# Kernel optimization log

Hardware: AMD Instinct MI355X
Metric: run time of the kernel (lower is better)

## Reference

```python
import jax, jax.numpy as jnp
import numpy as np

# scipy.ndimage.gaussian_filter(sigma=1, truncate=4): radius 4, 9-tap kernel on EVERY axis
_R = 4
_xk = np.arange(-_R, _R + 1)
_wk = np.exp(-0.5 * _xk * _xk)
_W1D = (_wk / _wk.sum()).astype(np.float32)


def _sym_idx(n, r):
    # scipy 'reflect' (symmetric, edge repeated) extension indices for any r, any n
    p = np.arange(-r, n + r)
    q = np.mod(p, 2 * n)
    return np.where(q < n, q, 2 * n - 1 - q)


def gauss_filter(x):
    # separable sigma=1 Gaussian over ALL axes (incl. batch & channel), as scipy does
    w = jnp.asarray(_W1D)
    for axis in range(x.ndim):
        n = x.shape[axis]
        idx = jnp.asarray(_sym_idx(n, _R))
        xp = jnp.take(x, idx, axis=axis)  # symmetric-padded along `axis`
        acc = w[0] * jax.lax.slice_in_dim(xp, 0, n, axis=axis)
        for k in range(1, 2 * _R + 1):
            acc = acc + w[k] * jax.lax.slice_in_dim(xp, k, k + n, axis=axis)
        x = acc
    return x


def downsample(x):
    return x[:, :, ::2, ::2, ::2]


def upsample(x):
    # faithful to source: zero-interleave D and H, but zeros are APPENDED along W
    B, C, D, H, W = x.shape
    t = jnp.stack([x, jnp.zeros_like(x)], axis=3).reshape(B, C, 2 * D, H, W)
    t = jnp.stack([t, jnp.zeros_like(t)], axis=4).reshape(B, C, 2 * D, 2 * H, W)
    t = jnp.concatenate([t, jnp.zeros_like(t)], axis=4)  # (B,C,2D,2H,2W), 2nd W-half zero
    return gauss_filter(t * 8.0)


def lap_pyramid(img, max_levels):
    pyr = []
    cur = img
    for _ in range(max_levels):
        filt = gauss_filter(cur)
        down = downsample(filt)
        up = upsample(down)
        pyr.append(cur - up)
        cur = down
    return pyr


def setup_inputs():
    key = jax.random.key(0)
    k1, k2 = jax.random.split(key)
    shape = (2, 1, 64, 256, 256)
    return {
        "input": jax.random.normal(k1, shape, dtype=jnp.float32),
        "target": jax.random.normal(k2, shape, dtype=jnp.float32),
    }


def reference(input, target):
    max_levels = 5
    pyr_in = lap_pyramid(input, max_levels)
    pyr_tg = lap_pyramid(target, max_levels)
    loss = jnp.float32(0.0)
    for a, b in zip(pyr_in, pyr_tg):
        loss = loss + jnp.mean(jnp.abs(a - b))  # F.l1_loss (mean reduction)
    return loss
```

## Files before the change

kernel.cpp:

```cpp
#include <hip/hip_runtime.h>
#include <hip/hip_bf16.h>
#include <math.h>


struct GW { float w[9]; float A, B; };

__device__ __forceinline__ int ridx(int p, int n) {
    int m = 2 * n;
    int q = (p + m) & (m - 1);
    return (q < n) ? q : (m - 1 - q);
}

__device__ __forceinline__ float block_sum256(float v) {
    #pragma unroll
    for (int off = 32; off > 0; off >>= 1) v += __shfl_down(v, off, 64);
    __shared__ float wp[4];
    int tid = threadIdx.x;
    if ((tid & 63) == 0) wp[tid >> 6] = v;
    __syncthreads();
    return wp[0] + wp[1] + wp[2] + wp[3];
}

template<bool WDIFF>
__global__ __launch_bounds__(256)
void k1l0(const float* __restrict__ in, const float* __restrict__ tg,
          float* __restrict__ T1, __hip_bfloat16* __restrict__ DIFF,
          float* __restrict__ P, GW g)
{
    const int H = 256, W = 256, Wd = 128;
    const int x0d = blockIdx.x * 64, y0d = blockIdx.y * 16, slice = blockIdx.z;
    __shared__ float raw[40][136];
    __shared__ float mid[40][64];
    const size_t in_off  = (size_t)slice * H * W;
    const size_t out_off = (size_t)slice * 128 * 128;
    const int tid = threadIdx.x;
    const int gy0 = 2*y0d - 4, gx0 = 2*x0d - 4;
    for (int i = tid; i < 40*32; i += 256) {
        int rr = i >> 5, c4 = (i & 31) + 1;
        int gy = ridx(gy0 + rr, H);
        size_t base = in_off + (size_t)gy * W + gx0 + 4*c4;
        float4 v = *(const float4*)(in + base);
        float4 b = *(const float4*)(tg + base);
        v.x -= b.x; v.y -= b.y; v.z -= b.z; v.w -= b.w;
        *(float4*)&raw[rr][4*c4] = v;
    }
    for (int i = tid; i < 40*8; i += 256) {
        int rr = i >> 3, j = i & 7;
        int cc = (j < 4) ? j : (128 + j);
        int gy = ridx(gy0 + rr, H);
        int gx = ridx(gx0 + cc, W);
        size_t idx = in_off + (size_t)gy * W + gx;
        raw[rr][cc] = in[idx] - tg[idx];
    }
    __syncthreads();
    if (WDIFF) {
        if (blockIdx.x == 0) {
            for (int i = tid; i < 32*128; i += 256) {
                int r = i >> 7, c = i & 127;
                DIFF[in_off + (size_t)(2*y0d + r) * W + c] =
                    __float2bfloat16(raw[4 + r][4 + c]);
            }
        } else {
            for (int i = tid; i < 32*4; i += 256) {
                int r = i >> 2, c = i & 3;
                DIFF[in_off + (size_t)(2*y0d + r) * W + 128 + c] =
                    __float2bfloat16(raw[4 + r][4 + c]);
            }
        }
    }
    if (blockIdx.x == 1) {
        float lsum = 0.f;
        for (int i = tid; i < 32*124; i += 256) {
            int r = i / 124, c = i - r*124;
            lsum += fabsf(raw[4 + r][8 + c]);
        }
        float tot = block_sum256(lsum);
        if (tid == 0)
            P[blockIdx.y + 8*blockIdx.z] = tot * (1.f / 8388608.f);
    }
    for (int i = tid; i < 40*64; i += 256) {
        int rr = i >> 6, c = i & 63;
        float s = 0.f;
        #pragma unroll
        for (int k = 0; k < 9; ++k) s = fmaf(g.w[k], raw[rr][2*c + k], s);
        mid[rr][c] = s;
    }
    __syncthreads();
    {
        int r = tid >> 6, c = tid & 63;
        int ox = x0d + c;
        #pragma unroll
        for (int j = 0; j < 4; ++j) {
            int oy = y0d + r*4 + j;
            int rb = 2*(r*4 + j);
            float s = 0.f;
            #pragma unroll
            for (int k = 0; k < 9; ++k) s = fmaf(g.w[k], mid[rb + k][c], s);
            T1[out_off + (size_t)oy * Wd + ox] = s;
        }
    }
}

__global__ __launch_bounds__(256)
void k2s(const float* __restrict__ Tin, float* __restrict__ Cout,
         int D, int Dd, int M4, GW g)
{
    long i = (long)blockIdx.x * 256 + threadIdx.x;
    if (i >= (long)Dd * M4) return;
    int zd = (int)(i / M4);
    int q  = (int)(i - (long)zd * M4);
    const float4* T = (const float4*)Tin;
    float4* O = (float4*)Cout;
    float4 s0 = {0,0,0,0}, s1 = {0,0,0,0};
    #pragma unroll
    for (int k = 0; k < 9; ++k) {
        int zp = 2*zd - 4 + k;
        int zk = (zp >= 0 && zp < D) ? zp : ridx(zp, D);
        float4 a = T[(size_t)zk * M4 + q];
        float4 b = T[(size_t)(D + zk) * M4 + q];
        s0.x = fmaf(g.w[k], a.x, s0.x); s0.y = fmaf(g.w[k], a.y, s0.y);
        s0.z = fmaf(g.w[k], a.z, s0.z); s0.w = fmaf(g.w[k], a.w, s0.w);
        s1.x = fmaf(g.w[k], b.x, s1.x); s1.y = fmaf(g.w[k], b.y, s1.y);
        s1.z = fmaf(g.w[k], b.z, s1.z); s1.w = fmaf(g.w[k], b.w, s1.w);
    }
    float4 o0, o1;
    o0.x = g.A*s0.x + g.B*s1.x; o0.y = g.A*s0.y + g.B*s1.y;
    o0.z = g.A*s0.z + g.B*s1.z; o0.w = g.A*s0.w + g.B*s1.w;
    o1.x = g.B*s0.x + g.A*s1.x; o1.y = g.B*s0.y + g.A*s1.y;
    o1.z = g.B*s0.z + g.A*s1.z; o1.w = g.B*s0.w + g.A*s1.w;
    O[(size_t)zd * M4 + q] = o0;
    O[(size_t)(Dd + zd) * M4 + q] = o1;
}

__device__ void dev_k1_slice(const float* __restrict__ inA, float* __restrict__ out,
                             int x0d, int y0d, int slice, int H, int W, int Hd, int Wd,
                             const GW& g)
{
    __shared__ float raw[40][136];
    __shared__ float mid[40][64];
    const size_t in_off  = (size_t)slice * H * W;
    const size_t out_off = (size_t)slice * Hd * Wd;
    const int tid = threadIdx.x;
    const int gy0 = 2*y0d - 4, gx0 = 2*x0d - 4;
    if (2*x0d + 127 < W) {
        for (int i = tid; i < 40*32; i += 256) {
            int rr = i >> 5, c4 = (i & 31) + 1;
            int gy = ridx(gy0 + rr, H);
            *(float4*)&raw[rr][4*c4] =
                *(const float4*)(inA + in_off + (size_t)gy * W + gx0 + 4*c4);
        }
        for (int i = tid; i < 40*8; i += 256) {
            int rr = i >> 3, j = i & 7;
            int cc = (j < 4) ? j : (128 + j);
            int gy = ridx(gy0 + rr, H), gx = ridx(gx0 + cc, W);
            raw[rr][cc] = inA[in_off + (size_t)gy * W + gx];
        }
    } else {
        for (int i = tid; i < 40*136; i += 256) {
            int rr = i / 136, cc = i - rr*136;
            int gy = ridx(gy0 + rr, H), gx = ridx(gx0 + cc, W);
            raw[rr][cc] = inA[in_off + (size_t)gy * W + gx];
        }
    }
    __syncthreads();
    for (int i = tid; i < 40*64; i += 256) {
        int rr = i >> 6, c = i & 63;
        float s = 0.f;
        #pragma unroll
        for (int k = 0; k < 9; ++k) s = fmaf(g.w[k], raw[rr][2*c + k], s);
        mid[rr][c] = s;
    }
    __syncthreads();
    {
        int r = tid >> 6, c = tid & 63;
        int ox = x0d + c;
        #pragma unroll
        for (int j = 0; j < 4; ++j) {
            int oy = y0d + r*4 + j;
            if (oy < Hd && ox < Wd) {
                int rb = 2*(r*4 + j);
                float s = 0.f;
                #pragma unroll
                for (int k = 0; k < 9; ++k) s = fmaf(g.w[k], mid[rb + k][c], s);
                out[out_off + (size_t)oy * Wd + ox] = s;
            }
        }
    }
}

__global__ __launch_bounds__(256)
void k1s(const float* __restrict__ inA, float* __restrict__ out,
         int H, int W, int Hd, int Wd, GW g)
{
    dev_k1_slice(inA, out, blockIdx.x*64, blockIdx.y*16, blockIdx.z, H, W, Hd, Wd, g);
}

__device__ void dev_k3_elem(long i, const float4* __restrict__ Dn, float4* __restrict__ O,
                            int D, int Dd, int M4, const GW& g)
{
    if (i >= (long)D * M4) return;
    int z = (int)(i / M4);
    int q = (int)(i - (long)z * M4);
    float4 s0 = {0,0,0,0}, s1 = {0,0,0,0};
    auto f4 = [](float4& a, float w, const float4 b) {
        a.x = fmaf(w, b.x, a.x); a.y = fmaf(w, b.y, a.y);
        a.z = fmaf(w, b.z, a.z); a.w = fmaf(w, b.w, a.w);
    };
    if (z >= 4 && z + 4 < D) {
        if ((z & 1) == 0) {
            int base = (z >> 1) - 2;
            #pragma unroll
            for (int kk = 0; kk < 5; ++kk) {
                f4(s0, g.w[2*kk], Dn[(size_t)(base + kk) * M4 + q]);
                f4(s1, g.w[2*kk], Dn[(size_t)(Dd + base + kk) * M4 + q]);
            }
        } else {
            int base = (z - 3) >> 1;
            #pragma unroll
            for (int kk = 0; kk < 4; ++kk) {
                f4(s0, g.w[2*kk+1], Dn[(size_t)(base + kk) * M4 + q]);
                f4(s1, g.w[2*kk+1], Dn[(size_t)(Dd + base + kk) * M4 + q]);
            }
        }
    } else {
        #pragma unroll
        for (int k = 0; k < 9; ++k) {
            int zk = ridx(z - 4 + k, D);
            if (!(zk & 1)) {
                int j = zk >> 1;
                f4(s0, g.w[k], Dn[(size_t)j * M4 + q]);
                f4(s1, g.w[k], Dn[(size_t)(Dd + j) * M4 + q]);
            }
        }
    }
    float4 o0, o1;
    o0.x = 8.f*(g.A*s0.x + g.B*s1.x); o0.y = 8.f*(g.A*s0.y + g.B*s1.y);
    o0.z = 8.f*(g.A*s0.z + g.B*s1.z); o0.w = 8.f*(g.A*s0.w + g.B*s1.w);
    o1.x = 8.f*(g.B*s0.x + g.A*s1.x); o1.y = 8.f*(g.B*s0.y + g.A*s1.y);
    o1.z = 8.f*(g.B*s0.z + g.A*s1.z); o1.w = 8.f*(g.B*s0.w + g.A*s1.w);
    O[(size_t)z * M4 + q] = o0;
    O[(size_t)(D + z) * M4 + q] = o1;
}

__global__ __launch_bounds__(256)
void fatk(const float* __restrict__ k1in, float* __restrict__ k1out,
          int H, int W, int Hd, int Wd, int nty, int n1,
          const float* __restrict__ dn, float* __restrict__ V,
          int D, int Dd, int M4, GW g)
{
    if ((int)blockIdx.x < n1) {
        int ty = (int)blockIdx.x % nty, slice = (int)blockIdx.x / nty;
        dev_k1_slice(k1in, k1out, 0, ty*16, slice, H, W, Hd, Wd, g);
    } else {
        long i = (long)((int)blockIdx.x - n1)*256 + threadIdx.x;
        dev_k3_elem(i, (const float4*)dn, (float4*)V, D, Dd, M4, g);
    }
}

struct K4P {
    const float* V[3];
    const float* dn34[2];
    const float* cur[5];
    const float* in; const float* tg;
    const __hip_bfloat16* DIFF;
    float* P;
    int use_diff;
    int bo[6];
    GW g;
};

__global__ __launch_bounds__(256)
void k4all(K4P p)
{
    const int Dt[5] = {64,32,16,8,4}, Ht[5] = {256,128,64,32,16};
    __shared__ float vt[20][72];
    __shared__ float mid[20][64];
    const int bid = (int)blockIdx.x;
    int l = 0;
    while (l < 4 && bid >= p.bo[l+1]) ++l;
    const int local = bid - p.bo[l];
    const int D = Dt[l], H = Ht[l], W = H;
    const int Dd = D >> 1, Hd = H >> 1, Wd = W >> 1, Md = Hd * Wd;
    const int ntx = (l == 0) ? 3 : ((W + 63) >> 6);
    const int nty = (H + 31) >> 5;
    const int s = local / (ntx*nty);
    const int rem = local - s*(ntx*nty);
    const int ty = rem / ntx, tx = rem - ty*ntx;
    const int x0 = tx*64, y0 = ty*32;
    const int b = s / D, z = s - b*D;
    const GW g = p.g;
    const int tid = threadIdx.x;
    const int vy0 = (y0 >> 1) - 2;

    if (l < 3) {
        const float* V = p.V[l];
        const size_t v_off = (size_t)s * Md;
        for (int i = tid; i < 20*72; i += 256) {
            int rr = i / 72, cc = i - rr*72;
            int vy = vy0 + rr;
            int txx = x0 - 4 + cc;
            if (txx < 0) txx = -1 - txx;
            float v = 0.f;
            if (vy >= 0 && vy < Hd && txx < Wd) v = V[v_off + (size_t)vy * Wd + txx];
            vt[rr][cc] = v;
        }
    } else {
        const float* dnb = p.dn34[l-3];
        const float* dn0 = dnb + (size_t)b * Dd * Md;
        const float* dn1 = dnb + (size_t)(1 - b) * Dd * Md;
        for (int i = tid; i < 20*72; i += 256) {
            int rr = i / 72, cc = i - rr*72;
            int vy = vy0 + rr;
            int txx = x0 - 4 + cc;
            if (txx < 0) txx = -1 - txx;
            float v = 0.f;
            if (vy >= 0 && vy < Hd && txx < Wd) {
                size_t o = (size_t)vy * Wd + txx;
                float s0 = 0.f, s1 = 0.f;
                #pragma unroll
                for (int k = 0; k < 9; ++k) {
                    int zk = ridx(z - 4 + k, D);
                    if (!(zk & 1)) {
                        int j = zk >> 1;
                        s0 = fmaf(g.w[k], dn0[(size_t)j * Md + o], s0);
                        s1 = fmaf(g.w[k], dn1[(size_t)j * Md + o], s1);
                    }
                }
                v = 8.f * (g.A*s0 + g.B*s1);
            }
            vt[rr][cc] = v;
        }
    }
    __syncthreads();
    for (int i = tid; i < 20*64; i += 256) {
        int rr = i >> 6, c = i & 63;
        float sv = 0.f;
        #pragma unroll
        for (int k = 0; k < 9; ++k) sv = fmaf(g.w[k], vt[rr][c + k], sv);
        mid[rr][c] = sv;
    }
    __syncthreads();
    const bool yin = (y0 >= 4) && (y0 + 35 < H);
    const int c = tid & 63;
    const int ry_base = (tid >> 6) * 8;
    const int ox = x0 + c;
    const int xlim = (l == 0) ? 132 : W;
    const size_t c_off = (size_t)s * H * W;
    const float* curl = (l >= 1) ? p.cur[l] : nullptr;
    float lsum = 0.f;
    #pragma unroll
    for (int j = 0; j < 8; ++j) {
        int ry = ry_base + j;
        int oy = y0 + ry;
        if (ox < xlim && oy < H) {
            float sv = 0.f;
            if (yin) {
                if (!(j & 1)) {
                    int r0 = ry >> 1;
                    sv = g.w[0]*mid[r0][c] + g.w[2]*mid[r0+1][c] + g.w[4]*mid[r0+2][c]
                       + g.w[6]*mid[r0+3][c] + g.w[8]*mid[r0+4][c];
                } else {
                    int r0 = ((ry - 3) >> 1) + 2;
                    sv = g.w[1]*mid[r0][c] + g.w[3]*mid[r0+1][c]
                       + g.w[5]*mid[r0+2][c] + g.w[7]*mid[r0+3][c];
                }
            } else {
                #pragma unroll
                for (int k = 0; k < 9; ++k) {
                    int gy = ridx(oy - 4 + k, H);
                    if (!(gy & 1)) sv = fmaf(g.w[k], mid[(gy >> 1) - vy0][c], sv);
                }
            }
            size_t idx = c_off + (size_t)oy * W + ox;
            float cv;
            if (l == 0) cv = p.use_diff ? __bfloat162float(p.DIFF[idx])
                                        : (p.in[idx] - p.tg[idx]);
            else        cv = curl[idx];
            lsum += fabsf(cv - sv);
        }
    }
    float tot = block_sum256(lsum);
    if (tid == 0) p.P[1024 + bid] = tot / ((float)(2*D) * H * W);
}

__global__ __launch_bounds__(1024)
void kreduce(const float* __restrict__ P, int n, float* __restrict__ out)
{
    float s = 0.f;
    for (int i = threadIdx.x; i < n; i += 1024) s += P[i];
    #pragma unroll
    for (int off = 32; off > 0; off >>= 1) s += __shfl_down(s, off, 64);
    __shared__ float wp[16];
    if ((threadIdx.x & 63) == 0) wp[threadIdx.x >> 6] = s;
    __syncthreads();
    if (threadIdx.x == 0) {
        float t = 0.f;
        #pragma unroll
        for (int w = 0; w < 16; ++w) t += wp[w];
        out[0] = t;
    }
}

extern "C" void kernel_launch(void* const* d_in, const int* in_sizes, int n_in,
                              void* d_out, int out_size, void* d_ws, size_t ws_size,
                              hipStream_t stream)
{
    const float* in = (const float*)d_in[0];
    const float* tg = (const float*)d_in[1];
    float* out = (float*)d_out;

    GW g;
    {
        double u[9], S = 0.0;
        for (int k = 0; k < 9; ++k) { double d = k - 4; u[k] = exp(-0.5 * d * d); S += u[k]; }
        for (int k = 0; k < 9; ++k) g.w[k] = (float)(u[k] / S);
        g.A = (float)((2.0*u[0] + u[1] + u[3] + u[4]) / S);
        g.B = (float)((u[1] + 2.0*u[2] + u[3]) / S);
    }

    float* T1  = (float*)d_ws;
    float* C1  = T1  + 2097152;
    float* C2  = C1  + 1048576;
    float* C3  = C2  + 131072;
    float* C4  = C3  + 16384;
    float* C5  = C4  + 2048;
    float* Tl1 = C5  + 256;
    float* Tl2 = Tl1 + 262144;
    float* Tl3 = Tl2 + 32768;
    float* Tl4 = Tl3 + 4096;
    float* V0  = Tl4 + 512;
    float* V1  = V0  + 2097152;
    float* V2  = V1  + 262144;
    float* P   = V2  + 32768;
    float* wend = P + 8192;
    __hip_bfloat16* DIFF = (__hip_bfloat16*)wend;
    const size_t base_bytes = (size_t)((char*)wend - (char*)d_ws);
    const size_t diff_bytes = (size_t)2 * 64 * 256 * 256 * sizeof(__hip_bfloat16);
    const int use_diff = (ws_size >= base_bytes + diff_bytes) ? 1 : 0;

    dim3 blk(256);

    if (use_diff) k1l0<true ><<<dim3(2,8,128), blk, 0, stream>>>(in, tg, T1, DIFF, P, g);
    else          k1l0<false><<<dim3(2,8,128), blk, 0, stream>>>(in, tg, T1, nullptr, P, g);

    k2s<<<dim3(512), blk, 0, stream>>>(T1, C1, 64, 32, 4096, g);

    fatk<<<dim3(256 + 1024), blk, 0, stream>>>(C1, Tl1, 128, 128, 64, 64, 4, 256,
                                               C1, V0, 64, 32, 4096, g);
    k2s<<<dim3(64), blk, 0, stream>>>(Tl1, C2, 32, 16, 1024, g);

    fatk<<<dim3(64 + 128), blk, 0, stream>>>(C2, Tl2, 64, 64, 32, 32, 2, 64,
                                             C2, V1, 32, 16, 1024, g);
    k2s<<<dim3(8), blk, 0, stream>>>(Tl2, C3, 16, 8, 256, g);

    fatk<<<dim3(16 + 16), blk, 0, stream>>>(C3, Tl3, 32, 32, 16, 16, 1, 16,
                                            C3, V2, 16, 8, 256, g);
    k2s<<<dim3(1), blk, 0, stream>>>(Tl3, C4, 8, 4, 64, g);

    k1s<<<dim3(1,1,8), blk, 0, stream>>>(C4, Tl4, 16, 16, 8, 8, g);
    k2s<<<dim3(1), blk, 0, stream>>>(Tl4, C5, 4, 2, 16, g);

    K4P prm;
    prm.V[0] = V0; prm.V[1] = V1; prm.V[2] = V2;
    prm.dn34[0] = C4; prm.dn34[1] = C5;
    prm.cur[0] = nullptr; prm.cur[1] = C1; prm.cur[2] = C2; prm.cur[3] = C3; prm.cur[4] = C4;
    prm.in = in; prm.tg = tg;
    prm.DIFF = use_diff ? DIFF : nullptr;
    prm.P = P; prm.use_diff = use_diff;
    prm.g = g;
    prm.bo[0] = 0; prm.bo[1] = 3072; prm.bo[2] = 3584;
    prm.bo[3] = 3648; prm.bo[4] = 3664; prm.bo[5] = 3672;
    k4all<<<dim3(3672), blk, 0, stream>>>(prm);

    kreduce<<<1, 1024, 0, stream>>>(P, 1024 + 3672, out);
}
```

Measured before the change: 102.2 us.

## Fuse depth pass into next level's H/W filter and interleave loss blocks

Folds the separate depth/batch filter kernels (k2s) into the next level's in-plane filter kernel. Each block now computes the D-axis and batch-axis Gaussian while loading its tile, stores the downsampled level, and then runs the H/W passes. The per-level loss kernel is split into chunks that share launches with the later small stages, cutting the launch count and the serial dependency chain. The cost is redundant D-filter work on halo rows and scalar (non-float4) strided loads, and the merged kernels use a larger shared-memory footprint, which can lower occupancy for the loss blocks.

```diff
diff --git a/kernel.cpp b/kernel.cpp
--- a/kernel.cpp
+++ b/kernel.cpp
@@ -101,103 +101,77 @@
     }
 }
 
-__global__ __launch_bounds__(256)
-void k2s(const float* __restrict__ Tin, float* __restrict__ Cout,
-         int D, int Dd, int M4, GW g)
-{
-    long i = (long)blockIdx.x * 256 + threadIdx.x;
-    if (i >= (long)Dd * M4) return;
-    int zd = (int)(i / M4);
-    int q  = (int)(i - (long)zd * M4);
-    const float4* T = (const float4*)Tin;
-    float4* O = (float4*)Cout;
-    float4 s0 = {0,0,0,0}, s1 = {0,0,0,0};
-    #pragma unroll
-    for (int k = 0; k < 9; ++k) {
-        int zp = 2*zd - 4 + k;
-        int zk = (zp >= 0 && zp < D) ? zp : ridx(zp, D);
-        float4 a = T[(size_t)zk * M4 + q];
-        float4 b = T[(size_t)(D + zk) * M4 + q];
-        s0.x = fmaf(g.w[k], a.x, s0.x); s0.y = fmaf(g.w[k], a.y, s0.y);
-        s0.z = fmaf(g.w[k], a.z, s0.z); s0.w = fmaf(g.w[k], a.w, s0.w);
-        s1.x = fmaf(g.w[k], b.x, s1.x); s1.y = fmaf(g.w[k], b.y, s1.y);
-        s1.z = fmaf(g.w[k], b.z, s1.z); s1.w = fmaf(g.w[k], b.w, s1.w);
-    }
-    float4 o0, o1;
-    o0.x = g.A*s0.x + g.B*s1.x; o0.y = g.A*s0.y + g.B*s1.y;
-    o0.z = g.A*s0.z + g.B*s1.z; o0.w = g.A*s0.w + g.B*s1.w;
-    o1.x = g.B*s0.x + g.A*s1.x; o1.y = g.B*s0.y + g.A*s1.y;
-    o1.z = g.B*s0.z + g.A*s1.z; o1.w = g.B*s0.w + g.A*s1.w;
-    O[(size_t)zd * M4 + q] = o0;
-    O[(size_t)(Dd + zd) * M4 + q] = o1;
-}
-
-__device__ void dev_k1_slice(const float* __restrict__ inA, float* __restrict__ out,
-                             int x0d, int y0d, int slice, int H, int W, int Hd, int Wd,
-                             const GW& g)
-{
-    __shared__ float raw[40][136];
-    __shared__ float mid[40][64];
-    const size_t in_off  = (size_t)slice * H * W;
-    const size_t out_off = (size_t)slice * Hd * Wd;
+struct MP {
+    const float* Tin; float* C; float* Tout;
+    int Dz, Dc, Hp, Wp, nty, writeT, nM;
+};
+
+__device__ void dev_M(int m, const MP& mp, const GW& g, float* smem)
+{
+    float* raw = smem;
+    float* mid = smem + 40*136;
     const int tid = threadIdx.x;
-    const int gy0 = 2*y0d - 4, gx0 = 2*x0d - 4;
-    if (2*x0d + 127 < W) {
-        for (int i = tid; i < 40*32; i += 256) {
-            int rr = i >> 5, c4 = (i & 31) + 1;
-            int gy = ridx(gy0 + rr, H);
-            *(float4*)&raw[rr][4*c4] =
-                *(const float4*)(inA + in_off + (size_t)gy * W + gx0 + 4*c4);
-        }
-        for (int i = tid; i < 40*8; i += 256) {
-            int rr = i >> 3, j = i & 7;
-            int cc = (j < 4) ? j : (128 + j);
-            int gy = ridx(gy0 + rr, H), gx = ridx(gx0 + cc, W);
-            raw[rr][cc] = inA[in_off + (size_t)gy * W + gx];
-        }
-    } else {
-        for (int i = tid; i < 40*136; i += 256) {
-            int rr = i / 136, cc = i - rr*136;
-            int gy = ridx(gy0 + rr, H), gx = ridx(gx0 + cc, W);
-            raw[rr][cc] = inA[in_off + (size_t)gy * W + gx];
-        }
-    }
+    const int ytile = m % mp.nty;
+    const int zidx  = m / mp.nty;
+    const int b  = zidx / mp.Dc;
+    const int zc = zidx - b * mp.Dc;
+    const int Dz = mp.Dz, Hp = mp.Hp, Wp = mp.Wp;
+    const int Hd = Hp >> 1, Wd = Wp >> 1;
+    const int y0d = ytile * 16;
+    const int CC = (Wp + 8 > 136) ? 136 : (Wp + 8);
+    const size_t plane = (size_t)Hp * Wp;
+    for (int i = tid; i < 40*CC; i += 256) {
+        int rr = i / CC, cc = i - rr*CC;
+        int gy = ridx(2*y0d - 4 + rr, Hp);
+        int gx = ridx(cc - 4, Wp);
+        size_t base = (size_t)gy * Wp + gx;
+        float s0 = 0.f, s1 = 0.f;
+        #pragma unroll
+        for (int k = 0; k < 9; ++k) {
+            int zt = ridx(2*zc - 4 + k, Dz);
+            s0 = fmaf(g.w[k], mp.Tin[(size_t)zt * plane + base], s0);
+            s1 = fmaf(g.w[k], mp.Tin[(size_t)(Dz + zt) * plane + base], s1);
+        }
+        float val = (b == 0) ? (g.A*s0 + g.B*s1) : (g.B*s0 + g.A*s1);
+        raw[rr*136 + cc] = val;
+        int gyo = 2*y0d + rr - 4;
+        if (rr >= 4 && rr < 36 && gyo < Hp && cc >= 4 && cc < 4 + Wp) {
+            mp.C[((size_t)(b*mp.Dc + zc) * Hp + gyo) * Wp + (cc - 4)] = val;
+        }
+    }
+    if (!mp.writeT) return;
     __syncthreads();
     for (int i = tid; i < 40*64; i += 256) {
         int rr = i >> 6, c = i & 63;
         float s = 0.f;
         #pragma unroll
-        for (int k = 0; k < 9; ++k) s = fmaf(g.w[k], raw[rr][2*c + k], s);
-        mid[rr][c] = s;
+        for (int k = 0; k < 9; ++k) s = fmaf(g.w[k], raw[rr*136 + 2*c + k], s);
+        mid[rr*64 + c] = s;
     }
     __syncthreads();
     {
         int r = tid >> 6, c = tid & 63;
-        int ox = x0d + c;
         #pragma unroll
         for (int j = 0; j < 4; ++j) {
             int oy = y0d + r*4 + j;
-            if (oy < Hd && ox < Wd) {
+            if (oy < Hd && c < Wd) {
                 int rb = 2*(r*4 + j);
                 float s = 0.f;
                 #pragma unroll
-                for (int k = 0; k < 9; ++k) s = fmaf(g.w[k], mid[rb + k][c], s);
-                out[out_off + (size_t)oy * Wd + ox] = s;
-            }
-        }
-    }
-}
-
-__global__ __launch_bounds__(256)
-void k1s(const float* __restrict__ inA, float* __restrict__ out,
-         int H, int W, int Hd, int Wd, GW g)
-{
-    dev_k1_slice(inA, out, blockIdx.x*64, blockIdx.y*16, blockIdx.z, H, W, Hd, Wd, g);
-}
-
-__device__ void dev_k3_elem(long i, const float4* __restrict__ Dn, float4* __restrict__ O,
-                            int D, int Dd, int M4, const GW& g)
-{
+                for (int k = 0; k < 9; ++k) s = fmaf(g.w[k], mid[(rb+k)*64 + c], s);
+                mp.Tout[((size_t)(b*mp.Dc + zc) * Hd + oy) * Wd + c] = s;
+            }
+        }
+    }
+}
+
+struct K3 { const float* dn; float* V; int D, Dd, M4, n; };
+
+__device__ void dev_k3_elem(long i, const K3& kp, const GW& g)
+{
+    const float4* Dn = (const float4*)kp.dn;
+    float4* O = (float4*)kp.V;
+    const int D = kp.D, Dd = kp.Dd, M4 = kp.M4;
     if (i >= (long)D * M4) return;
     int z = (int)(i / M4);
     int q = (int)(i - (long)z * M4);
@@ -242,21 +216,6 @@
     O[(size_t)(D + z) * M4 + q] = o1;
 }
 
-__global__ __launch_bounds__(256)
-void fatk(const float* __restrict__ k1in, float* __restrict__ k1out,
-          int H, int W, int Hd, int Wd, int nty, int n1,
-          const float* __restrict__ dn, float* __restrict__ V,
-          int D, int Dd, int M4, GW g)
-{
-    if ((int)blockIdx.x < n1) {
-        int ty = (int)blockIdx.x % nty, slice = (int)blockIdx.x / nty;
-        dev_k1_slice(k1in, k1out, 0, ty*16, slice, H, W, Hd, Wd, g);
-    } else {
-        long i = (long)((int)blockIdx.x - n1)*256 + threadIdx.x;
-        dev_k3_elem(i, (const float4*)dn, (float4*)V, D, Dd, M4, g);
-    }
-}
-
 struct K4P {
     const float* V[3];
     const float* dn34[2];
@@ -269,16 +228,14 @@
     GW g;
 };
 
-__global__ __launch_bounds__(256)
-void k4all(K4P p)
+__device__ void dev_k4(int gbid, const K4P& p, float* smem)
 {
     const int Dt[5] = {64,32,16,8,4}, Ht[5] = {256,128,64,32,16};
-    __shared__ float vt[20][72];
-    __shared__ float mid[20][64];
-    const int bid = (int)blockIdx.x;
+    float* vt  = smem;
+    float* mid = smem + 20*72;
     int l = 0;
-    while (l < 4 && bid >= p.bo[l+1]) ++l;
-    const int local = bid - p.bo[l];
+    while (l < 4 && gbid >= p.bo[l+1]) ++l;
+    const int local = gbid - p.bo[l];
     const int D = Dt[l], H = Ht[l], W = H;
     const int Dd = D >> 1, Hd = H >> 1, Wd = W >> 1, Md = Hd * Wd;
     const int ntx = (l == 0) ? 3 : ((W + 63) >> 6);
@@ -302,7 +259,7 @@
             if (txx < 0) txx = -1 - txx;
             float v = 0.f;
             if (vy >= 0 && vy < Hd && txx < Wd) v = V[v_off + (size_t)vy * Wd + txx];
-            vt[rr][cc] = v;
+            vt[rr*72 + cc] = v;
         }
     } else {
         const float* dnb = p.dn34[l-3];
@@ -328,7 +285,7 @@
                 }
                 v = 8.f * (g.A*s0 + g.B*s1);
             }
-            vt[rr][cc] = v;
+            vt[rr*72 + cc] = v;
         }
     }
     __syncthreads();
@@ -336,8 +293,8 @@
         int rr = i >> 6, c = i & 63;
         float sv = 0.f;
         #pragma unroll
-        for (int k = 0; k < 9; ++k) sv = fmaf(g.w[k], vt[rr][c + k], sv);
-        mid[rr][c] = sv;
+        for (int k = 0; k < 9; ++k) sv = fmaf(g.w[k], vt[rr*72 + c + k], sv);
+        mid[rr*64 + c] = sv;
     }
     __syncthreads();
     const bool yin = (y0 >= 4) && (y0 + 35 < H);
@@ -357,18 +314,19 @@
             if (yin) {
                 if (!(j & 1)) {
                     int r0 = ry >> 1;
-                    sv = g.w[0]*mid[r0][c] + g.w[2]*mid[r0+1][c] + g.w[4]*mid[r0+2][c]
-                       + g.w[6]*mid[r0+3][c] + g.w[8]*mid[r0+4][c];
+                    sv = g.w[0]*mid[r0*64+c] + g.w[2]*mid[(r0+1)*64+c]
+                       + g.w[4]*mid[(r0+2)*64+c] + g.w[6]*mid[(r0+3)*64+c]
+                       + g.w[8]*mid[(r0+4)*64+c];
                 } else {
                     int r0 = ((ry - 3) >> 1) + 2;
-                    sv = g.w[1]*mid[r0][c] + g.w[3]*mid[r0+1][c]
-                       + g.w[5]*mid[r0+2][c] + g.w[7]*mid[r0+3][c];
+                    sv = g.w[1]*mid[r0*64+c] + g.w[3]*mid[(r0+1)*64+c]
+                       + g.w[5]*mid[(r0+2)*64+c] + g.w[7]*mid[(r0+3)*64+c];
                 }
             } else {
                 #pragma unroll
                 for (int k = 0; k < 9; ++k) {
                     int gy = ridx(oy - 4 + k, H);
-                    if (!(gy & 1)) sv = fmaf(g.w[k], mid[(gy >> 1) - vy0][c], sv);
+                    if (!(gy & 1)) sv = fmaf(g.w[k], mid[((gy >> 1) - vy0)*64 + c], sv);
                 }
             }
             size_t idx = c_off + (size_t)oy * W + ox;
@@ -380,7 +338,50 @@
         }
     }
     float tot = block_sum256(lsum);
-    if (tid == 0) p.P[1024 + bid] = tot / ((float)(2*D) * H * W);
+    if (tid == 0) p.P[1024 + gbid] = tot / ((float)(2*D) * H * W);
+}
+
+__global__ __launch_bounds__(256)
+void kM1(MP mp, GW g)
+{
+    __shared__ float smem[40*136 + 40*64];
+    dev_M((int)blockIdx.x, mp, g, smem);
+}
+
+__global__ __launch_bounds__(256)
+void kD3(MP mp, K3 k3, GW g)
+{
+    __shared__ float smem[40*136 + 40*64];
+    int bid = (int)blockIdx.x;
+    if (bid < mp.nM) dev_M(bid, mp, g, smem);
+    else dev_k3_elem((long)(bid - mp.nM)*256 + threadIdx.x, k3, g);
+}
+
+__global__ __launch_bounds__(256)
+void kD45(MP mp, K3 k3, K4P k4, int bid0, GW g)
+{
+    __shared__ float smem[40*136 + 40*64];
+    int bid = (int)blockIdx.x;
+    if (bid < mp.nM) dev_M(bid, mp, g, smem);
+    else if (bid < mp.nM + k3.n)
+        dev_k3_elem((long)(bid - mp.nM)*256 + threadIdx.x, k3, g);
+    else dev_k4(bid0 + (bid - mp.nM - k3.n), k4, smem);
+}
+
+__global__ __launch_bounds__(256)
+void kD6(MP mp, K4P k4, int bid0, GW g)
+{
+    __shared__ float smem[40*136 + 40*64];
+    int bid = (int)blockIdx.x;
+    if (bid < mp.nM) dev_M(bid, mp, g, smem);
+    else dev_k4(bid0 + (bid - mp.nM), k4, smem);
+}
+
+__global__ __launch_bounds__(256)
+void kD7(K4P k4, int bid0)
+{
+    __shared__ float smem[20*72 + 20*64];
+    dev_k4(bid0 + (int)blockIdx.x, k4, smem);
 }
 
 __global__ __launch_bounds__(1024)
@@ -440,37 +441,54 @@
 
     dim3 blk(256);
 
+    K4P k4;
+    k4.V[0] = V0; k4.V[1] = V1; k4.V[2] = V2;
+    k4.dn34[0] = C4; k4.dn34[1] = C5;
+    k4.cur[0] = nullptr; k4.cur[1] = C1; k4.cur[2] = C2; k4.cur[3] = C3; k4.cur[4] = C4;
+    k4.in = in; k4.tg = tg;
+    k4.DIFF = use_diff ? DIFF : nullptr;
+    k4.P = P; k4.use_diff = use_diff;
+    k4.g = g;
+    k4.bo[0] = 0; k4.bo[1] = 3072; k4.bo[2] = 3584;
+    k4.bo[3] = 3648; k4.bo[4] = 3664; k4.bo[5] = 3672;
+
     if (use_diff) k1l0<true ><<<dim3(2,8,128), blk, 0, stream>>>(in, tg, T1, DIFF, P, g);
     else          k1l0<false><<<dim3(2,8,128), blk, 0, stream>>>(in, tg, T1, nullptr, P, g);
 
-    k2s<<<dim3(512), blk, 0, stream>>>(T1, C1, 64, 32, 4096, g);
-
-    fatk<<<dim3(256 + 1024), blk, 0, stream>>>(C1, Tl1, 128, 128, 64, 64, 4, 256,
-                                               C1, V0, 64, 32, 4096, g);
-    k2s<<<dim3(64), blk, 0, stream>>>(Tl1, C2, 32, 16, 1024, g);
-
-    fatk<<<dim3(64 + 128), blk, 0, stream>>>(C2, Tl2, 64, 64, 32, 32, 2, 64,
-                                             C2, V1, 32, 16, 1024, g);
-    k2s<<<dim3(8), blk, 0, stream>>>(Tl2, C3, 16, 8, 256, g);
-
-    fatk<<<dim3(16 + 16), blk, 0, stream>>>(C3, Tl3, 32, 32, 16, 16, 1, 16,
-                                            C3, V2, 16, 8, 256, g);
-    k2s<<<dim3(1), blk, 0, stream>>>(Tl3, C4, 8, 4, 64, g);
-
-    k1s<<<dim3(1,1,8), blk, 0, stream>>>(C4, Tl4, 16, 16, 8, 8, g);
-    k2s<<<dim3(1), blk, 0, stream>>>(Tl4, C5, 4, 2, 16, g);
-
-    K4P prm;
-    prm.V[0] = V0; prm.V[1] = V1; prm.V[2] = V2;
-    prm.dn34[0] = C4; prm.dn34[1] = C5;
-    prm.cur[0] = nullptr; prm.cur[1] = C1; prm.cur[2] = C2; prm.cur[3] = C3; prm.cur[4] = C4;
-    prm.in = in; prm.tg = tg;
-    prm.DIFF = use_diff ? DIFF : nullptr;
-    prm.P = P; prm.use_diff = use_diff;
-    prm.g = g;
-    prm.bo[0] = 0; prm.bo[1] = 3072; prm.bo[2] = 3584;
-    prm.bo[3] = 3648; prm.bo[4] = 3664; prm.bo[5] = 3672;
-    k4all<<<dim3(3672), blk, 0, stream>>>(prm);
+    {
+        MP mp; mp.Tin = T1; mp.C = C1; mp.Tout = Tl1;
+        mp.Dz = 64; mp.Dc = 32; mp.Hp = 128; mp.Wp = 128; mp.nty = 4; mp.writeT = 1;
+        mp.nM = 256;
+        kM1<<<dim3(256), blk, 0, stream>>>(mp, g);
+    }
+    {
+        MP mp; mp.Tin = Tl1; mp.C = C2; mp.Tout = Tl2;
+        mp.Dz = 32; mp.Dc = 16; mp.Hp = 64; mp.Wp = 64; mp.nty = 2; mp.writeT = 1;
+        mp.nM = 64;
+        K3 k3 = { C1, V0, 64, 32, 4096, 1024 };
+        kD3<<<dim3(64 + 1024), blk, 0, stream>>>(mp, k3, g);
+    }
+    {
+        MP mp; mp.Tin = Tl2; mp.C = C3; mp.Tout = Tl3;
+        mp.Dz = 16; mp.Dc = 8; mp.Hp = 32; mp.Wp = 32; mp.nty = 1; mp.writeT = 1;
+        mp.nM = 16;
+        K3 k3 = { C2, V1, 32, 16, 1024, 128 };
+        kD45<<<dim3(16 + 128 + 3072), blk, 0, stream>>>(mp, k3, k4, 0, g);
+    }
+    {
+        MP mp; mp.Tin = Tl3; mp.C = C4; mp.Tout = Tl4;
+        mp.Dz = 8; mp.Dc = 4; mp.Hp = 16; mp.Wp = 16; mp.nty = 1; mp.writeT = 1;
+        mp.nM = 8;
+        K3 k3 = { C3, V2, 16, 8, 256, 16 };
+        kD45<<<dim3(8 + 16 + 512), blk, 0, stream>>>(mp, k3, k4, 3072, g);
+    }
+    {
+        MP mp; mp.Tin = Tl4; mp.C = C5; mp.Tout = nullptr;
+        mp.Dz = 4; mp.Dc = 2; mp.Hp = 8; mp.Wp = 8; mp.nty = 1; mp.writeT = 0;
+        mp.nM = 4;
+        kD6<<<dim3(4 + 64), blk, 0, stream>>>(mp, k4, 3584, g);
+    }
+    kD7<<<dim3(24), blk, 0, stream>>>(k4, 3648);
 
     kreduce<<<1, 1024, 0, stream>>>(P, 1024 + 3672, out);
 }
```

Result: slower. 128.8 us (+26.0%).

## Restructure pyramid schedule: fuse level losses into producer kernels and single-block tail

Applied to the files above, without the earlier changes.

The launch sequence is reorganised so each level's loss computation runs in the same launch as the next level's filtering. Levels 1-2 compute the z-upsample directly from the downsampled data instead of materialising V1/V2, and all of levels 3-4 are collapsed into one 1024-thread block working from shared memory. This cuts the kernel launch count and the intermediate global traffic, and lets the large level-0 loss overlap with the small level-1 z-pass. In exchange, the tail runs serially on a single block, and levels 1-2 recompute the z-upsample per tile, including over halo rows.

```diff
diff --git a/kernel.cpp b/kernel.cpp
--- a/kernel.cpp
+++ b/kernel.cpp
@@ -19,6 +19,21 @@
     if ((tid & 63) == 0) wp[tid >> 6] = v;
     __syncthreads();
     return wp[0] + wp[1] + wp[2] + wp[3];
+}
+
+__device__ __forceinline__ float block_sum1024(float v) {
+    #pragma unroll
+    for (int off = 32; off > 0; off >>= 1) v += __shfl_down(v, off, 64);
+    __shared__ float wp[16];
+    int tid = threadIdx.x;
+    if ((tid & 63) == 0) wp[tid >> 6] = v;
+    __syncthreads();
+    float t = 0.f;
+    if (tid == 0) {
+        #pragma unroll
+        for (int w = 0; w < 16; ++w) t += wp[w];
+    }
+    return t;
 }
 
 template<bool WDIFF>
@@ -101,16 +116,12 @@
     }
 }
 
-__global__ __launch_bounds__(256)
-void k2s(const float* __restrict__ Tin, float* __restrict__ Cout,
-         int D, int Dd, int M4, GW g)
-{
-    long i = (long)blockIdx.x * 256 + threadIdx.x;
+__device__ void dev_k2_elem(long i, const float4* __restrict__ T, float4* __restrict__ O,
+                            int D, int Dd, int M4, const GW& g)
+{
     if (i >= (long)Dd * M4) return;
     int zd = (int)(i / M4);
     int q  = (int)(i - (long)zd * M4);
-    const float4* T = (const float4*)Tin;
-    float4* O = (float4*)Cout;
     float4 s0 = {0,0,0,0}, s1 = {0,0,0,0};
     #pragma unroll
     for (int k = 0; k < 9; ++k) {
@@ -130,6 +141,14 @@
     o1.z = g.B*s0.z + g.A*s1.z; o1.w = g.B*s0.w + g.A*s1.w;
     O[(size_t)zd * M4 + q] = o0;
     O[(size_t)(Dd + zd) * M4 + q] = o1;
+}
+
+__global__ __launch_bounds__(256)
+void k2s(const float* __restrict__ Tin, float* __restrict__ Cout,
+         int D, int Dd, int M4, GW g)
+{
+    long i = (long)blockIdx.x * 256 + threadIdx.x;
+    dev_k2_elem(i, (const float4*)Tin, (float4*)Cout, D, Dd, M4, g);
 }
 
 __device__ void dev_k1_slice(const float* __restrict__ inA, float* __restrict__ out,
@@ -186,13 +205,6 @@
             }
         }
     }
-}
-
-__global__ __launch_bounds__(256)
-void k1s(const float* __restrict__ inA, float* __restrict__ out,
-         int H, int W, int Hd, int Wd, GW g)
-{
-    dev_k1_slice(inA, out, blockIdx.x*64, blockIdx.y*16, blockIdx.z, H, W, Hd, Wd, g);
 }
 
 __device__ void dev_k3_elem(long i, const float4* __restrict__ Dn, float4* __restrict__ O,
@@ -242,72 +254,136 @@
     O[(size_t)(D + z) * M4 + q] = o1;
 }
 
-__global__ __launch_bounds__(256)
-void fatk(const float* __restrict__ k1in, float* __restrict__ k1out,
-          int H, int W, int Hd, int Wd, int nty, int n1,
-          const float* __restrict__ dn, float* __restrict__ V,
-          int D, int Dd, int M4, GW g)
-{
-    if ((int)blockIdx.x < n1) {
-        int ty = (int)blockIdx.x % nty, slice = (int)blockIdx.x / nty;
-        dev_k1_slice(k1in, k1out, 0, ty*16, slice, H, W, Hd, Wd, g);
-    } else {
-        long i = (long)((int)blockIdx.x - n1)*256 + threadIdx.x;
-        dev_k3_elem(i, (const float4*)dn, (float4*)V, D, Dd, M4, g);
-    }
-}
-
-struct K4P {
-    const float* V[3];
-    const float* dn34[2];
-    const float* cur[5];
-    const float* in; const float* tg;
-    const __hip_bfloat16* DIFF;
-    float* P;
-    int use_diff;
-    int bo[6];
-    GW g;
-};
-
-__global__ __launch_bounds__(256)
-void k4all(K4P p)
-{
-    const int Dt[5] = {64,32,16,8,4}, Ht[5] = {256,128,64,32,16};
+__device__ void dev_k4v0(int local, const float* __restrict__ V0,
+                         const __hip_bfloat16* __restrict__ DIFF,
+                         const float* __restrict__ in, const float* __restrict__ tg,
+                         int use_diff, float* __restrict__ P, const GW& g)
+{
     __shared__ float vt[20][72];
     __shared__ float mid[20][64];
-    const int bid = (int)blockIdx.x;
-    int l = 0;
-    while (l < 4 && bid >= p.bo[l+1]) ++l;
-    const int local = bid - p.bo[l];
-    const int D = Dt[l], H = Ht[l], W = H;
-    const int Dd = D >> 1, Hd = H >> 1, Wd = W >> 1, Md = Hd * Wd;
-    const int ntx = (l == 0) ? 3 : ((W + 63) >> 6);
-    const int nty = (H + 31) >> 5;
+    const int H = 256, W = 256, Hd = 128, Wd = 128, Md = 128*128;
+    const int s = local / 24;
+    const int rem = local - s*24;
+    const int ty = rem / 3, tx = rem - ty*3;
+    const int x0 = tx*64, y0 = ty*32;
+    const int tid = threadIdx.x;
+    const int vy0 = (y0 >> 1) - 2;
+    const size_t v_off = (size_t)s * Md;
+    for (int i = tid; i < 20*72; i += 256) {
+        int rr = i / 72, cc = i - rr*72;
+        int vy = vy0 + rr;
+        int txx = x0 - 4 + cc;
+        if (txx < 0) txx = -1 - txx;
+        float v = 0.f;
+        if (vy >= 0 && vy < Hd && txx < Wd) v = V0[v_off + (size_t)vy * Wd + txx];
+        vt[rr][cc] = v;
+    }
+    __syncthreads();
+    for (int i = tid; i < 20*64; i += 256) {
+        int rr = i >> 6, c = i & 63;
+        float sv = 0.f;
+        #pragma unroll
+        for (int k = 0; k < 9; ++k) sv = fmaf(g.w[k], vt[rr][c + k], sv);
+        mid[rr][c] = sv;
+    }
+    __syncthreads();
+    const bool yin = (y0 >= 4) && (y0 + 35 < H);
+    const int c = tid & 63;
+    const int ry_base = (tid >> 6) * 8;
+    const int ox = x0 + c;
+    const size_t c_off = (size_t)s * H * W;
+    float lsum = 0.f;
+    #pragma unroll
+    for (int j = 0; j < 8; ++j) {
+        int ry = ry_base + j;
+        int oy = y0 + ry;
+        if (ox < 132 && oy < H) {
+            float sv = 0.f;
+            if (yin) {
+                if (!(j & 1)) {
+                    int r0 = ry >> 1;
+                    sv = g.w[0]*mid[r0][c] + g.w[2]*mid[r0+1][c] + g.w[4]*mid[r0+2][c]
+                       + g.w[6]*mid[r0+3][c] + g.w[8]*mid[r0+4][c];
+                } else {
+                    int r0 = ((ry - 3) >> 1) + 2;
+                    sv = g.w[1]*mid[r0][c] + g.w[3]*mid[r0+1][c]
+                       + g.w[5]*mid[r0+2][c] + g.w[7]*mid[r0+3][c];
+                }
+            } else {
+                #pragma unroll
+                for (int k = 0; k < 9; ++k) {
+                    int gy = ridx(oy - 4 + k, H);
+                    if (!(gy & 1)) sv = fmaf(g.w[k], mid[(gy >> 1) - vy0][c], sv);
+                }
+            }
+            size_t idx = c_off + (size_t)oy * W + ox;
+            float cv = use_diff ? __bfloat162float(DIFF[idx]) : (in[idx] - tg[idx]);
+            lsum += fabsf(cv - sv);
+        }
+    }
+    float tot = block_sum256(lsum);
+    if (tid == 0) P[1024 + local] = tot * (1.f / 8388608.f);
+}
+
+__device__ void dev_k4f(int local, const float* __restrict__ dnb,
+                        const float* __restrict__ cur, float* __restrict__ Pslot,
+                        int D, int H, int ntx, int nty, float invn, const GW& g)
+{
+    __shared__ float vt[20][72];
+    __shared__ float mid[20][64];
+    const int W = H, Dd = D >> 1, Hd = H >> 1, Wd = W >> 1, Md = Hd * Wd;
     const int s = local / (ntx*nty);
     const int rem = local - s*(ntx*nty);
     const int ty = rem / ntx, tx = rem - ty*ntx;
     const int x0 = tx*64, y0 = ty*32;
     const int b = s / D, z = s - b*D;
-    const GW g = p.g;
+    const float* dn0 = dnb + (size_t)b * Dd * Md;
+    const float* dn1 = dnb + (size_t)(1 - b) * Dd * Md;
     const int tid = threadIdx.x;
     const int vy0 = (y0 >> 1) - 2;
 
-    if (l < 3) {
-        const float* V = p.V[l];
-        const size_t v_off = (size_t)s * Md;
+    const bool zin = (z >= 4) && (z + 4 < D);
+    if (zin && !(z & 1)) {
+        const int j0 = (z >> 1) - 2;
         for (int i = tid; i < 20*72; i += 256) {
             int rr = i / 72, cc = i - rr*72;
             int vy = vy0 + rr;
             int txx = x0 - 4 + cc;
             if (txx < 0) txx = -1 - txx;
             float v = 0.f;
-            if (vy >= 0 && vy < Hd && txx < Wd) v = V[v_off + (size_t)vy * Wd + txx];
+            if (vy >= 0 && vy < Hd && txx < Wd) {
+                size_t o = (size_t)vy * Wd + txx;
+                float s0 = 0.f, s1 = 0.f;
+                #pragma unroll
+                for (int t = 0; t < 5; ++t) {
+                    s0 = fmaf(g.w[2*t], dn0[(size_t)(j0 + t) * Md + o], s0);
+                    s1 = fmaf(g.w[2*t], dn1[(size_t)(j0 + t) * Md + o], s1);
+                }
+                v = 8.f * (g.A*s0 + g.B*s1);
+            }
             vt[rr][cc] = v;
         }
+    } else if (zin) {
+        const int j0 = (z - 3) >> 1;
+        for (int i = tid; i < 20*72; i += 256) {
+            int rr = i / 72, cc = i - rr*72;
+            int vy = vy0 + rr;
+            int txx = x0 - 4 + cc;
+            if (txx < 0) txx = -1 - txx;
+            float v = 0.f;
+            if (vy >= 0 && vy < Hd && txx < Wd) {
+                size_t o = (size_t)vy * Wd + txx;
+                float s0 = 0.f, s1 = 0.f;
+                #pragma unroll
+                for (int t = 0; t < 4; ++t) {
+                    s0 = fmaf(g.w[2*t+1], dn0[(size_t)(j0 + t) * Md + o], s0);
+                    s1 = fmaf(g.w[2*t+1], dn1[(size_t)(j0 + t) * Md + o], s1);
+                }
+                v = 8.f * (g.A*s0 + g.B*s1);
+            }
+            vt[rr][cc] = v;
+        }
     } else {
-        const float* dnb = p.dn34[l-3];
-        const float* dn0 = dnb + (size_t)b * Dd * Md;
-        const float* dn1 = dnb + (size_t)(1 - b) * Dd * Md;
         for (int i = tid; i < 20*72; i += 256) {
             int rr = i / 72, cc = i - rr*72;
             int vy = vy0 + rr;
@@ -344,15 +420,13 @@
     const int c = tid & 63;
     const int ry_base = (tid >> 6) * 8;
     const int ox = x0 + c;
-    const int xlim = (l == 0) ? 132 : W;
     const size_t c_off = (size_t)s * H * W;
-    const float* curl = (l >= 1) ? p.cur[l] : nullptr;
     float lsum = 0.f;
     #pragma unroll
     for (int j = 0; j < 8; ++j) {
         int ry = ry_base + j;
         int oy = y0 + ry;
-        if (ox < xlim && oy < H) {
+        if (ox < W && oy < H) {
             float sv = 0.f;
             if (yin) {
                 if (!(j & 1)) {
@@ -371,16 +445,196 @@
                     if (!(gy & 1)) sv = fmaf(g.w[k], mid[(gy >> 1) - vy0][c], sv);
                 }
             }
-            size_t idx = c_off + (size_t)oy * W + ox;
-            float cv;
-            if (l == 0) cv = p.use_diff ? __bfloat162float(p.DIFF[idx])
-                                        : (p.in[idx] - p.tg[idx]);
-            else        cv = curl[idx];
-            lsum += fabsf(cv - sv);
+            lsum += fabsf(cur[c_off + (size_t)oy * W + ox] - sv);
         }
     }
     float tot = block_sum256(lsum);
-    if (tid == 0) p.P[1024 + bid] = tot / ((float)(2*D) * H * W);
+    if (tid == 0) Pslot[local] = tot * invn;
+}
+
+__global__ __launch_bounds__(256)
+void kD3(const float* __restrict__ C1, float* __restrict__ Tl1,
+         float* __restrict__ V0, GW g)
+{
+    int bid = (int)blockIdx.x;
+    if (bid < 256) {
+        int ty = bid & 3, slice = bid >> 2;
+        dev_k1_slice(C1, Tl1, 0, ty*16, slice, 128, 128, 64, 64, g);
+    } else {
+        long i = (long)(bid - 256)*256 + threadIdx.x;
+        dev_k3_elem(i, (const float4*)C1, (float4*)V0, 64, 32, 4096, g);
+    }
+}
+
+__global__ __launch_bounds__(256)
+void kD4(const float* __restrict__ Tl1, float* __restrict__ C2,
+         const float* __restrict__ V0, const __hip_bfloat16* __restrict__ DIFF,
+         const float* __restrict__ in, const float* __restrict__ tg,
+         int use_diff, float* __restrict__ P, GW g)
+{
+    int bid = (int)blockIdx.x;
+    if (bid < 64) {
+        long i = (long)bid*256 + threadIdx.x;
+        dev_k2_elem(i, (const float4*)Tl1, (float4*)C2, 32, 16, 1024, g);
+    } else {
+        dev_k4v0(bid - 64, V0, DIFF, in, tg, use_diff, P, g);
+    }
+}
+
+__global__ __launch_bounds__(256)
+void kD5(const float* __restrict__ C2, float* __restrict__ Tl2,
+         const float* __restrict__ C1, float* __restrict__ P, GW g)
+{
+    int bid = (int)blockIdx.x;
+    if (bid < 64) {
+        int ty = bid & 1, slice = bid >> 1;
+        dev_k1_slice(C2, Tl2, 0, ty*16, slice, 64, 64, 32, 32, g);
+    } else {
+        dev_k4f(bid - 64, C2, C1, P + 1024 + 3072, 32, 128, 2, 4,
+                1.f / 1048576.f, g);
+    }
+}
+
+__global__ __launch_bounds__(256)
+void kD7(const float* __restrict__ C3, float* __restrict__ Tl3,
+         const float* __restrict__ C2, float* __restrict__ P, GW g)
+{
+    int bid = (int)blockIdx.x;
+    if (bid < 16) {
+        dev_k1_slice(C3, Tl3, 0, 0, bid, 32, 32, 16, 16, g);
+    } else {
+        dev_k4f(bid - 16, C3, C2, P + 1024 + 3584, 16, 64, 1, 2,
+                1.f / 131072.f, g);
+    }
+}
+
+__global__ __launch_bounds__(1024)
+void megatail(const float* __restrict__ Tl3g, const float* __restrict__ C3g,
+              float* __restrict__ P, GW g)
+{
+    __shared__ float sTl3[4096];
+    __shared__ float sC4[2048];
+    __shared__ float sTl4[512];
+    __shared__ float sC5[256];
+    __shared__ float sV3[4096];
+    __shared__ float sV4[512];
+    const int tid = threadIdx.x;
+    for (int i = tid; i < 4096; i += 1024) sTl3[i] = Tl3g[i];
+    __syncthreads();
+    for (int i = tid; i < 2048; i += 1024) {
+        int slice = i >> 8, yx = i & 255;
+        int b = slice >> 2, zc = slice & 3;
+        float s0 = 0.f, s1 = 0.f;
+        #pragma unroll
+        for (int k = 0; k < 9; ++k) {
+            int zk = ridx(2*zc - 4 + k, 8);
+            s0 = fmaf(g.w[k], sTl3[zk*256 + yx], s0);
+            s1 = fmaf(g.w[k], sTl3[(8 + zk)*256 + yx], s1);
+        }
+        sC4[i] = (b == 0) ? (g.A*s0 + g.B*s1) : (g.B*s0 + g.A*s1);
+    }
+    __syncthreads();
+    for (int i = tid; i < 512; i += 1024) {
+        int slice = i >> 6, y = (i >> 3) & 7, x = i & 7;
+        float s = 0.f;
+        for (int ky = 0; ky < 9; ++ky) {
+            int gy = ridx(2*y - 4 + ky, 16);
+            float rs = 0.f;
+            #pragma unroll
+            for (int kx = 0; kx < 9; ++kx) {
+                int gx = ridx(2*x - 4 + kx, 16);
+                rs = fmaf(g.w[kx], sC4[slice*256 + gy*16 + gx], rs);
+            }
+            s = fmaf(g.w[ky], rs, s);
+        }
+        sTl4[i] = s;
+    }
+    __syncthreads();
+    for (int i = tid; i < 256; i += 1024) {
+        int slice = i >> 6, yx = i & 63;
+        int b = slice >> 1, zc = slice & 1;
+        float s0 = 0.f, s1 = 0.f;
+        #pragma unroll
+        for (int k = 0; k < 9; ++k) {
+            int zk = ridx(2*zc - 4 + k, 4);
+            s0 = fmaf(g.w[k], sTl4[zk*64 + yx], s0);
+            s1 = fmaf(g.w[k], sTl4[(4 + zk)*64 + yx], s1);
+        }
+        sC5[i] = (b == 0) ? (g.A*s0 + g.B*s1) : (g.B*s0 + g.A*s1);
+    }
+    __syncthreads();
+    for (int i = tid; i < 4096; i += 1024) {
+        int slice = i >> 8, yx = i & 255;
+        int b = slice >> 3, z = slice & 7;
+        float s0 = 0.f, s1 = 0.f;
+        #pragma unroll
+        for (int k = 0; k < 9; ++k) {
+            int zk = ridx(z - 4 + k, 8);
+            if (!(zk & 1)) {
+                int j = zk >> 1;
+                s0 = fmaf(g.w[k], sC4[j*256 + yx], s0);
+                s1 = fmaf(g.w[k], sC4[(4 + j)*256 + yx], s1);
+            }
+        }
+        sV3[i] = (b == 0) ? 8.f*(g.A*s0 + g.B*s1) : 8.f*(g.B*s0 + g.A*s1);
+    }
+    for (int i = tid; i < 512; i += 1024) {
+        int slice = i >> 6, yx = i & 63;
+        int b = slice >> 2, z = slice & 3;
+        float s0 = 0.f, s1 = 0.f;
+        #pragma unroll
+        for (int k = 0; k < 9; ++k) {
+            int zk = ridx(z - 4 + k, 4);
+            if (!(zk & 1)) {
+                int j = zk >> 1;
+                s0 = fmaf(g.w[k], sC5[j*64 + yx], s0);
+                s1 = fmaf(g.w[k], sC5[(2 + j)*64 + yx], s1);
+            }
+        }
+        sV4[i] = (b == 0) ? 8.f*(g.A*s0 + g.B*s1) : 8.f*(g.B*s0 + g.A*s1);
+    }
+    __syncthreads();
+    float lsum = 0.f;
+    for (int i = tid; i < 16384; i += 1024) {
+        int slice = i >> 10, y = (i >> 5) & 31, x = i & 31;
+        float up = 0.f;
+        for (int ky = 0; ky < 9; ++ky) {
+            int gy = ridx(y - 4 + ky, 32);
+            if (gy & 1) continue;
+            int vy = gy >> 1;
+            float rs = 0.f;
+            #pragma unroll
+            for (int kx = 0; kx < 9; ++kx) {
+                int txx = x - 4 + kx;
+                if (txx < 0) txx = -1 - txx;
+                float v = (txx < 16) ? sV3[slice*256 + vy*16 + txx] : 0.f;
+                rs = fmaf(g.w[kx], v, rs);
+            }
+            up = fmaf(g.w[ky], rs, up);
+        }
+        lsum += fabsf(C3g[slice*1024 + y*32 + x] - up) * (1.f / 16384.f);
+    }
+    for (int i = tid; i < 2048; i += 1024) {
+        int slice = i >> 8, y = (i >> 4) & 15, x = i & 15;
+        float up = 0.f;
+        for (int ky = 0; ky < 9; ++ky) {
+            int gy = ridx(y - 4 + ky, 16);
+            if (gy & 1) continue;
+            int vy = gy >> 1;
+            float rs = 0.f;
+            #pragma unroll
+            for (int kx = 0; kx < 9; ++kx) {
+                int txx = x - 4 + kx;
+                if (txx < 0) txx = -1 - txx;
+                float v = (txx < 8) ? sV4[slice*64 + vy*8 + txx] : 0.f;
+                rs = fmaf(g.w[kx], v, rs);
+            }
+            up = fmaf(g.w[ky], rs, up);
+        }
+        lsum += fabsf(sC4[slice*256 + y*16 + x] - up) * (1.f / 2048.f);
+    }
+    float tot = block_sum1024(lsum);
+    if (tid == 0) P[4672] = tot;
 }
 
 __global__ __launch_bounds__(1024)
@@ -388,17 +642,8 @@
 {
     float s = 0.f;
     for (int i = threadIdx.x; i < n; i += 1024) s += P[i];
-    #pragma unroll
-    for (int off = 32; off > 0; off >>= 1) s += __shfl_down(s, off, 64);
-    __shared__ float wp[16];
-    if ((threadIdx.x & 63) == 0) wp[threadIdx.x >> 6] = s;
-    __syncthreads();
-    if (threadIdx.x == 0) {
-        float t = 0.f;
-        #pragma unroll
-        for (int w = 0; w < 16; ++w) t += wp[w];
-        out[0] = t;
-    }
+    float t = block_sum1024(s);
+    if (threadIdx.x == 0) out[0] = t;
 }
 
 extern "C" void kernel_launch(void* const* d_in, const int* in_sizes, int n_in,
@@ -422,16 +667,11 @@
     float* C1  = T1  + 2097152;
     float* C2  = C1  + 1048576;
     float* C3  = C2  + 131072;
-    float* C4  = C3  + 16384;
-    float* C5  = C4  + 2048;
-    float* Tl1 = C5  + 256;
+    float* Tl1 = C3  + 16384;
     float* Tl2 = Tl1 + 262144;
     float* Tl3 = Tl2 + 32768;
-    float* Tl4 = Tl3 + 4096;
-    float* V0  = Tl4 + 512;
-    float* V1  = V0  + 2097152;
-    float* V2  = V1  + 262144;
-    float* P   = V2  + 32768;
+    float* V0  = Tl3 + 4096;
+    float* P   = V0  + 2097152;
     float* wend = P + 8192;
     __hip_bfloat16* DIFF = (__hip_bfloat16*)wend;
     const size_t base_bytes = (size_t)((char*)wend - (char*)d_ws);
@@ -445,32 +685,18 @@
 
     k2s<<<dim3(512), blk, 0, stream>>>(T1, C1, 64, 32, 4096, g);
 
-    fatk<<<dim3(256 + 1024), blk, 0, stream>>>(C1, Tl1, 128, 128, 64, 64, 4, 256,
-                                               C1, V0, 64, 32, 4096, g);
-    k2s<<<dim3(64), blk, 0, stream>>>(Tl1, C2, 32, 16, 1024, g);
-
-    fatk<<<dim3(64 + 128), blk, 0, stream>>>(C2, Tl2, 64, 64, 32, 32, 2, 64,
-                                             C2, V1, 32, 16, 1024, g);
+    kD3<<<dim3(1280), blk, 0, stream>>>(C1, Tl1, V0, g);
+
+    kD4<<<dim3(3136), blk, 0, stream>>>(Tl1, C2, V0, use_diff ? DIFF : nullptr,
+                                        in, tg, use_diff, P, g);
+
+    kD5<<<dim3(576), blk, 0, stream>>>(C2, Tl2, C1, P, g);
+
     k2s<<<dim3(8), blk, 0, stream>>>(Tl2, C3, 16, 8, 256, g);
 
-    fatk<<<dim3(16 + 16), blk, 0, stream>>>(C3, Tl3, 32, 32, 16, 16, 1, 16,
-                                            C3, V2, 16, 8, 256, g);
-    k2s<<<dim3(1), blk, 0, stream>>>(Tl3, C4, 8, 4, 64, g);
-
-    k1s<<<dim3(1,1,8), blk, 0, stream>>>(C4, Tl4, 16, 16, 8, 8, g);
-    k2s<<<dim3(1), blk, 0, stream>>>(Tl4, C5, 4, 2, 16, g);
-
-    K4P prm;
-    prm.V[0] = V0; prm.V[1] = V1; prm.V[2] = V2;
-    prm.dn34[0] = C4; prm.dn34[1] = C5;
-    prm.cur[0] = nullptr; prm.cur[1] = C1; prm.cur[2] = C2; prm.cur[3] = C3; prm.cur[4] = C4;
-    prm.in = in; prm.tg = tg;
-    prm.DIFF = use_diff ? DIFF : nullptr;
-    prm.P = P; prm.use_diff = use_diff;
-    prm.g = g;
-    prm.bo[0] = 0; prm.bo[1] = 3072; prm.bo[2] = 3584;
-    prm.bo[3] = 3648; prm.bo[4] = 3664; prm.bo[5] = 3672;
-    k4all<<<dim3(3672), blk, 0, stream>>>(prm);
-
-    kreduce<<<1, 1024, 0, stream>>>(P, 1024 + 3672, out);
-}
+    kD7<<<dim3(80), blk, 0, stream>>>(C3, Tl3, C2, P, g);
+
+    megatail<<<dim3(1), dim3(1024), 0, stream>>>(Tl3, C3, P, g);
+
+    kreduce<<<dim3(1), dim3(1024), 0, stream>>>(P, 4673, out);
+}
```

Result: slower. 134.2 us (+31.3%).
